# Kernel optimization log

Measured on AMD Instinct MI355X. Metric: run time of the kernel, lower is better.

The kernel has to match this reference:

```python
import jax, jax.numpy as jnp
from jax import lax
import numpy as np

MAX_SELECT = 100
NMS_THRESH = 0.1
LINES_PER_BLOCK = 4
CHARS_PER_LINE = 1
BELONG_THRESH = 0.6
SCORE_THRESH = 0.1
SAMPLE_NUM = 10


def cxcywh_to_xyxy(b):
    cx, cy, w, h = jnp.split(b, 4, axis=-1)
    return jnp.concatenate([cx - 0.5 * w, cy - 0.5 * h, cx + 0.5 * w, cy + 0.5 * h], axis=-1)


def bezier_aabb(cp):
    # cp: [K, 8, 2] control points (two cubic beziers: top 0:4, bottom 4:8)
    t = jnp.linspace(0.0, 1.0, SAMPLE_NUM)[:, None]      # [S,1]
    ti = 1.0 - t
    basis = jnp.concatenate([ti ** 3, 3 * t * ti ** 2, 3 * t ** 2 * ti, t ** 3], axis=-1)  # [S,4]
    top = jnp.einsum('sf,kfd->ksd', basis, cp[:, 0:4, :])
    bot = jnp.einsum('sf,kfd->ksd', basis, cp[:, 4:8, :])
    pts = jnp.concatenate([top, bot], axis=1)            # [K, 2S, 2]
    return jnp.concatenate([pts.min(axis=1), pts.max(axis=1)], axis=-1)  # [K,4] = x1,y1,x2,y2


def nms_keep_mask(boxes, init_keep, thresh):
    # boxes already sorted by descending score (topk order); returns keep mask
    K = boxes.shape[0]
    area = (boxes[:, 2] - boxes[:, 0]) * (boxes[:, 3] - boxes[:, 1])
    tl = jnp.maximum(boxes[:, None, :2], boxes[None, :, :2])
    br = jnp.minimum(boxes[:, None, 2:], boxes[None, :, 2:])
    wh = jnp.clip(br - tl, 0.0)
    inter = wh[..., 0] * wh[..., 1]
    iou = inter / (area[:, None] + area[None, :] - inter)
    idx = jnp.arange(K)

    def body(keep, i):
        sup = (iou[i] > thresh) & (idx > i) & keep[i]
        return keep & ~sup, None

    keep, _ = lax.scan(body, init_keep, jnp.arange(K))
    return keep


def filter_image(probs, raw, tsize, parent_raw, ef, is_bezier):
    # probs: [N], raw: [N, 4 or 16], tsize: [2] = (h, w)
    img_h, img_w = tsize[0], tsize[1]
    scale_box = jnp.stack([img_w, img_h, img_w, img_h])
    K = MAX_SELECT
    vals, sidx = lax.top_k(probs, K)
    keep = vals > SCORE_THRESH
    keep = jnp.where(keep.any(), keep, jnp.arange(K) == 0)

    if is_bezier:
        scale_pts = jnp.tile(tsize, 8)                    # [h,w]*8, matches repeat(8)
        ctrl = (raw[sidx] * scale_pts).reshape(K, 8, 2)
        boxes = bezier_aabb(ctrl)
        data = ctrl
    else:
        data = cxcywh_to_xyxy(raw[sidx]) * scale_box
        boxes = data

    if parent_raw is not None:
        pbox = cxcywh_to_xyxy(parent_raw[sidx // ef]) * scale_box
        ix1 = jnp.maximum(boxes[:, 0], pbox[:, 0])
        iy1 = jnp.maximum(boxes[:, 1], pbox[:, 1])
        ix2 = jnp.minimum(boxes[:, 2], pbox[:, 2])
        iy2 = jnp.minimum(boxes[:, 3], pbox[:, 3])
        inter = jnp.clip(ix2 - ix1, 0.0) * jnp.clip(iy2 - iy1, 0.0)
        carea = (boxes[:, 2] - boxes[:, 0]) * (boxes[:, 3] - boxes[:, 1])
        belong = inter / (carea + 1e-6)
        valid = belong > BELONG_THRESH
        fb = jnp.arange(K) == jnp.argmax(jnp.where(keep, belong, -jnp.inf))
        valid = jnp.where((valid & keep).any(), valid, fb)
        mask = keep & valid
    else:
        maxs = jnp.stack([img_w, img_h, img_w, img_h])
        data = jnp.clip(data, 0.0, maxs)
        boxes = data
        mask = keep

    nk = nms_keep_mask(lax.stop_gradient(boxes), mask, NMS_THRESH)
    if is_bezier:
        data = data.reshape(K, 16)
    data = jnp.where(nk[:, None], data, 0.0)
    scores = jnp.where(nk, vals, 0.0)
    return data, scores, nk


def _probs(logits):
    return jax.nn.sigmoid(logits)[..., 0]


def reference(pred_block_logits, pred_line_logits, pred_char_logits,
              pred_block, pred_line, pred_char, target_sizes):
    bp = _probs(pred_block_logits)
    lp = _probs(pred_line_logits)
    cp = _probs(pred_char_logits)
    blk = jax.vmap(lambda p, r, t: filter_image(p, r, t, None, 1, False))(bp, pred_block, target_sizes)
    lin = jax.vmap(lambda p, r, pr, t: filter_image(p, r, t, pr, LINES_PER_BLOCK, False))(lp, pred_line, pred_block, target_sizes)
    chr_ = jax.vmap(lambda p, r, pr, t: filter_image(p, r, t, pr, CHARS_PER_LINE, True))(cp, pred_char, pred_line, target_sizes)
    # padded outputs: (data, scores, keep_mask) per level; invalid rows are zeroed
    return (*blk, *lin, *chr_)


def setup_inputs() -> dict:
    key = jax.random.key(0)
    ks = jax.random.split(key, 7)
    B, NB, NL, NC = 64, 4096, 16384, 16384
    return {
        'pred_block_logits': jax.random.normal(ks[0], (B, NB, 1), jnp.float32),
        'pred_line_logits': jax.random.normal(ks[1], (B, NL, 1), jnp.float32),
        'pred_char_logits': jax.random.normal(ks[2], (B, NC, 1), jnp.float32),
        'pred_block': jax.random.uniform(ks[3], (B, NB, 4), jnp.float32),
        'pred_line': jax.random.uniform(ks[4], (B, NL, 4), jnp.float32),
        'pred_char': jax.random.uniform(ks[5], (B, NC, 16), jnp.float32),
        'target_sizes': 512.0 + 1024.0 * jax.random.uniform(ks[6], (B, 2), jnp.float32),
    }
```

## Files before the change

kernel.cpp:

```cpp
#include <hip/hip_runtime.h>
#include <math.h>

#define NTHREADS 256
#define KSEL 100
#define NBINS 2048
#define CAP 1024
#define SCORE_TH 0.1f
#define NMS_TH 0.1f
#define BELONG_TH 0.6f

typedef unsigned long long ull;

__device__ __forceinline__ ull make_key(float f, unsigned gidx) {
    unsigned u = __float_as_uint(f);
    u = (u & 0x80000000u) ? ~u : (u | 0x80000000u);
    return (((ull)u) << 32) | (ull)(0xFFFFFFFFu - gidx);
}
__device__ __forceinline__ float key_val(ull k) {
    unsigned u = (unsigned)(k >> 32);
    u = (u & 0x80000000u) ? (u ^ 0x80000000u) : ~u;
    return __uint_as_float(u);
}
__device__ __forceinline__ unsigned key_idx(ull k) {
    return 0xFFFFFFFFu - (unsigned)(k & 0xFFFFFFFFu);
}
__device__ __forceinline__ int binof(float p) {
    int b = (int)(p * (float)NBINS);
    b = b < 0 ? 0 : (b > NBINS - 1 ? NBINS - 1 : b);
    return b;
}

struct SharedMem {
    union {
        unsigned hist[NBINS];
        ull cand[CAP];
        ull part[4];
    } u;
    int bstar;
    int scnt;
    int wsum[4];
    float prob[KSEL];
    int   sidx[KSEL];
    float box[KSEL][4];
    float data16[KSEL][16];
    float area[KSEL];
    float belong[KSEL];
    unsigned char keep[KSEL];
    unsigned char valid[KSEL];
    unsigned char nk[KSEL];
    int argm;
    int anyvk;
};

template <int NPT, bool IS_BEZIER, bool HAS_PARENT>
__device__ void filter_impl(SharedMem* sm,
                            const float* __restrict__ logits,
                            const float* __restrict__ raw,
                            const float* __restrict__ parent_raw,
                            const float* __restrict__ tsizes,
                            float* __restrict__ out_data,
                            float* __restrict__ out_scores,
                            float* __restrict__ out_keep,
                            int img, int N, int PN, int ef) {
    const int tid = threadIdx.x;
    const int lane = tid & 63;
    const int wv = tid >> 6;
    const float* lg = logits + (size_t)img * N;

    for (int i = tid; i < NBINS; i += NTHREADS) sm->u.hist[i] = 0;
    if (tid == 0) sm->scnt = 0;
    __syncthreads();

    float p[NPT];
#pragma unroll
    for (int j = 0; j < NPT; ++j) {
        float x = lg[j * NTHREADS + tid];
        p[j] = 1.0f / (1.0f + expf(-x));
    }

#pragma unroll
    for (int j = 0; j < NPT; ++j)
        atomicAdd(&sm->u.hist[binof(p[j])], 1u);
    __syncthreads();

    int c[8];
    int s = 0;
#pragma unroll
    for (int q = 0; q < 8; ++q) {
        c[q] = (int)sm->u.hist[NBINS - 1 - 8 * tid - q];
        s += c[q];
    }
    int vv = s;
#pragma unroll
    for (int off = 1; off < 64; off <<= 1) {
        int o = __shfl_up(vv, off, 64);
        if (lane >= off) vv += o;
    }
    if (lane == 63) sm->wsum[wv] = vv;
    __syncthreads();
    int base = 0;
    for (int u2 = 0; u2 < wv; ++u2) base += sm->wsum[u2];
    int run = base + vv - s;
#pragma unroll
    for (int q = 0; q < 8; ++q) {
        int before = run;
        run += c[q];
        if (before < KSEL && run >= KSEL) sm->bstar = NBINS - 1 - 8 * tid - q;
    }
    __syncthreads();
    const int bstar = sm->bstar;

#pragma unroll
    for (int j = 0; j < NPT; ++j) {
        if (binof(p[j]) >= bstar) {
            int pos = atomicAdd(&sm->scnt, 1);
            if (pos < CAP) sm->u.cand[pos] = make_key(p[j], (unsigned)(j * NTHREADS + tid));
        }
    }
    __syncthreads();
    const int cnt = sm->scnt;

    if (cnt <= CAP) {
        for (int t = tid; t < cnt; t += NTHREADS) {
            ull mk = sm->u.cand[t];
            int rank = 0;
            for (int u2 = 0; u2 < cnt; ++u2) rank += (sm->u.cand[u2] > mk) ? 1 : 0;
            if (rank < KSEL) {
                sm->prob[rank] = key_val(mk);
                sm->sidx[rank] = (int)key_idx(mk);
            }
        }
    } else {
        ull best = make_key(p[0], (unsigned)tid);
#pragma unroll
        for (int j = 1; j < NPT; ++j) {
            ull kk = make_key(p[j], (unsigned)(j * NTHREADS + tid));
            if (kk > best) best = kk;
        }
        for (int k = 0; k < KSEL; ++k) {
            ull m = best;
#pragma unroll
            for (int off = 32; off > 0; off >>= 1) {
                ull o = __shfl_down(m, off, 64);
                if (o > m) m = o;
            }
            if (lane == 0) sm->u.part[wv] = m;
            __syncthreads();
            ull w = sm->u.part[0];
#pragma unroll
            for (int q = 1; q < 4; ++q)
                if (sm->u.part[q] > w) w = sm->u.part[q];
            if (tid == 0) {
                sm->prob[k] = key_val(w);
                sm->sidx[k] = (int)key_idx(w);
            }
            __syncthreads();
            unsigned gidx = key_idx(w);
            if ((gidx & (NTHREADS - 1)) == (unsigned)tid) {
                int j = (int)(gidx >> 8);
#pragma unroll
                for (int jj = 0; jj < NPT; ++jj)
                    if (jj == j) p[jj] = -INFINITY;
                best = make_key(p[0], (unsigned)tid);
#pragma unroll
                for (int jj = 1; jj < NPT; ++jj) {
                    ull kk = make_key(p[jj], (unsigned)(jj * NTHREADS + tid));
                    if (kk > best) best = kk;
                }
            }
        }
    }
    __syncthreads();

    const float Himg = tsizes[img * 2 + 0];
    const float Wimg = tsizes[img * 2 + 1];

    if (tid < KSEL) {
        const int k = tid;
        const int si = sm->sidx[k];
        const float val = sm->prob[k];
        const bool any = sm->prob[0] > SCORE_TH;
        bool keep = any ? (val > SCORE_TH) : (k == 0);

        float bx1, by1, bx2, by2;
        if (IS_BEZIER) {
            const float* r = raw + ((size_t)img * N + si) * 16;
            float c16[16];
#pragma unroll
            for (int mm = 0; mm < 8; ++mm) {
                c16[2 * mm]     = r[2 * mm]     * Himg;
                c16[2 * mm + 1] = r[2 * mm + 1] * Wimg;
            }
            float mn0 = INFINITY, mn1 = INFINITY, mx0 = -INFINITY, mx1 = -INFINITY;
            const float step = 1.0f / 9.0f;
#pragma unroll
            for (int sNum = 0; sNum < 10; ++sNum) {
                float t = (float)sNum * step;
                float ti = 1.0f - t;
                float b0 = ti * ti * ti;
                float b1 = 3.0f * t * ti * ti;
                float b2 = 3.0f * t * t * ti;
                float b3 = t * t * t;
#pragma unroll
                for (int cu = 0; cu < 2; ++cu) {
                    const float* cc = c16 + cu * 8;
                    float p0 = b0 * cc[0] + b1 * cc[2] + b2 * cc[4] + b3 * cc[6];
                    float p1 = b0 * cc[1] + b1 * cc[3] + b2 * cc[5] + b3 * cc[7];
                    mn0 = fminf(mn0, p0); mx0 = fmaxf(mx0, p0);
                    mn1 = fminf(mn1, p1); mx1 = fmaxf(mx1, p1);
                }
            }
            bx1 = mn0; by1 = mn1; bx2 = mx0; by2 = mx1;
#pragma unroll
            for (int mm = 0; mm < 16; ++mm) sm->data16[k][mm] = c16[mm];
        } else {
            const float* r = raw + ((size_t)img * N + si) * 4;
            float cx = r[0], cy = r[1], w = r[2], h = r[3];
            bx1 = (cx - 0.5f * w) * Wimg;
            by1 = (cy - 0.5f * h) * Himg;
            bx2 = (cx + 0.5f * w) * Wimg;
            by2 = (cy + 0.5f * h) * Himg;
            if (!HAS_PARENT) {
                bx1 = fminf(fmaxf(bx1, 0.0f), Wimg);
                by1 = fminf(fmaxf(by1, 0.0f), Himg);
                bx2 = fminf(fmaxf(bx2, 0.0f), Wimg);
                by2 = fminf(fmaxf(by2, 0.0f), Himg);
            }
        }
        sm->box[k][0] = bx1; sm->box[k][1] = by1;
        sm->box[k][2] = bx2; sm->box[k][3] = by2;
        sm->area[k] = (bx2 - bx1) * (by2 - by1);
        sm->keep[k] = keep ? 1 : 0;

        if (HAS_PARENT) {
            int pi = si / ef;
            const float* pr = parent_raw + ((size_t)img * PN + pi) * 4;
            float pcx = pr[0], pcy = pr[1], pw = pr[2], ph = pr[3];
            float px1 = (pcx - 0.5f * pw) * Wimg;
            float py1 = (pcy - 0.5f * ph) * Himg;
            float px2 = (pcx + 0.5f * pw) * Wimg;
            float py2 = (pcy + 0.5f * ph) * Himg;
            float ix1 = fmaxf(bx1, px1), iy1 = fmaxf(by1, py1);
            float ix2 = fminf(bx2, px2), iy2 = fminf(by2, py2);
            float inter = fmaxf(ix2 - ix1, 0.0f) * fmaxf(iy2 - iy1, 0.0f);
            float carea = (bx2 - bx1) * (by2 - by1);
            float belong = inter / (carea + 1e-6f);
            sm->belong[k] = belong;
            sm->valid[k] = (belong > BELONG_TH) ? 1 : 0;
        }
    }
    __syncthreads();

    if (HAS_PARENT) {
        if (tid < 64) {
            ull k0 = make_key(sm->keep[tid] ? sm->belong[tid] : -INFINITY, (unsigned)tid);
            bool p0 = sm->valid[tid] && sm->keep[tid];
            ull k1 = 0;
            bool p1 = false;
            if (tid < KSEL - 64) {
                k1 = make_key(sm->keep[tid + 64] ? sm->belong[tid + 64] : -INFINITY,
                              (unsigned)(tid + 64));
                p1 = sm->valid[tid + 64] && sm->keep[tid + 64];
            }
            ull m = k0 > k1 ? k0 : k1;
#pragma unroll
            for (int off = 32; off > 0; off >>= 1) {
                ull o = __shfl_xor(m, off, 64);
                if (o > m) m = o;
            }
            ull bal = __ballot(p0 || p1);
            if (lane == 0) {
                sm->argm = (int)key_idx(m);
                sm->anyvk = (bal != 0ULL) ? 1 : 0;
            }
        }
        __syncthreads();
        if (tid < KSEL) {
            bool valid = sm->anyvk ? (sm->valid[tid] != 0) : (tid == sm->argm);
            sm->nk[tid] = (sm->keep[tid] && valid) ? 1 : 0;
        }
    } else {
        if (tid < KSEL) sm->nk[tid] = sm->keep[tid];
    }
    __syncthreads();

    if (tid < 64) {
        const int l = tid;
        float s0x1 = sm->box[l][0], s0y1 = sm->box[l][1];
        float s0x2 = sm->box[l][2], s0y2 = sm->box[l][3];
        float s0a = sm->area[l];
        float s1x1 = 0.f, s1y1 = 0.f, s1x2 = 0.f, s1y2 = 0.f, s1a = 0.f;
        if (l < KSEL - 64) {
            s1x1 = sm->box[l + 64][0]; s1y1 = sm->box[l + 64][1];
            s1x2 = sm->box[l + 64][2]; s1y2 = sm->box[l + 64][3];
            s1a = sm->area[l + 64];
        }
        ull keepLo = __ballot(sm->nk[l] != 0);
        ull keepHi = __ballot((l < KSEL - 64) && (sm->nk[l + 64] != 0));
        for (int i = 0; i < KSEL; ++i) {
            bool ki = (i < 64) ? (((keepLo >> i) & 1ULL) != 0)
                               : (((keepHi >> (i - 64)) & 1ULL) != 0);
            if (!ki) continue;
            float bx1, by1, bx2, by2, ba;
            if (i < 64) {
                bx1 = __shfl(s0x1, i, 64); by1 = __shfl(s0y1, i, 64);
                bx2 = __shfl(s0x2, i, 64); by2 = __shfl(s0y2, i, 64);
                ba = __shfl(s0a, i, 64);
            } else {
                int ii = i - 64;
                bx1 = __shfl(s1x1, ii, 64); by1 = __shfl(s1y1, ii, 64);
                bx2 = __shfl(s1x2, ii, 64); by2 = __shfl(s1y2, ii, 64);
                ba = __shfl(s1a, ii, 64);
            }
            float ix1 = fmaxf(bx1, s0x1), iy1 = fmaxf(by1, s0y1);
            float ix2 = fminf(bx2, s0x2), iy2 = fminf(by2, s0y2);
            float in0 = fmaxf(ix2 - ix1, 0.0f) * fmaxf(iy2 - iy1, 0.0f);
            float iou0 = in0 / (ba + s0a - in0);
            bool sup0 = (l > i) && (iou0 > NMS_TH);
            float jx1 = fmaxf(bx1, s1x1), jy1 = fmaxf(by1, s1y1);
            float jx2 = fminf(bx2, s1x2), jy2 = fminf(by2, s1y2);
            float in1 = fmaxf(jx2 - jx1, 0.0f) * fmaxf(jy2 - jy1, 0.0f);
            float iou1 = in1 / (ba + s1a - in1);
            bool sup1 = ((l + 64) > i) && (iou1 > NMS_TH);
            keepLo &= ~__ballot(sup0);
            keepHi &= ~__ballot(sup1);
        }
        sm->nk[l] = (unsigned char)((keepLo >> l) & 1ULL);
        if (l < KSEL - 64) sm->nk[l + 64] = (unsigned char)((keepHi >> l) & 1ULL);
    }
    __syncthreads();

    if (tid < KSEL) {
        const int k = tid;
        const bool nk = sm->nk[k] != 0;
        out_scores[(size_t)img * KSEL + k] = nk ? sm->prob[k] : 0.0f;
        out_keep[(size_t)img * KSEL + k] = nk ? 1.0f : 0.0f;
        if (IS_BEZIER) {
#pragma unroll
            for (int mm = 0; mm < 16; ++mm)
                out_data[((size_t)img * KSEL + k) * 16 + mm] = nk ? sm->data16[k][mm] : 0.0f;
        } else {
#pragma unroll
            for (int mm = 0; mm < 4; ++mm)
                out_data[((size_t)img * KSEL + k) * 4 + mm] = nk ? sm->box[k][mm] : 0.0f;
        }
    }
}

__global__ __launch_bounds__(NTHREADS) void postprocess_kernel(
    const float* __restrict__ blk_logits, const float* __restrict__ lin_logits,
    const float* __restrict__ chr_logits, const float* __restrict__ blk_raw,
    const float* __restrict__ lin_raw, const float* __restrict__ chr_raw,
    const float* __restrict__ tsizes, float* __restrict__ out) {
    __shared__ SharedMem sm;
    const int b = blockIdx.x;
    const int level = b >> 6;
    const int img = b & 63;

    float* blk_data = out + 0;
    float* blk_sc   = out + 25600;
    float* blk_kp   = out + 32000;
    float* lin_data = out + 38400;
    float* lin_sc   = out + 64000;
    float* lin_kp   = out + 70400;
    float* chr_data = out + 76800;
    float* chr_sc   = out + 179200;
    float* chr_kp   = out + 185600;

    if (level == 0) {
        filter_impl<16, false, false>(&sm, blk_logits, blk_raw, nullptr, tsizes,
                                      blk_data, blk_sc, blk_kp, img, 4096, 0, 1);
    } else if (level == 1) {
        filter_impl<64, false, true>(&sm, lin_logits, lin_raw, blk_raw, tsizes,
                                     lin_data, lin_sc, lin_kp, img, 16384, 4096, 4);
    } else {
        filter_impl<64, true, true>(&sm, chr_logits, chr_raw, lin_raw, tsizes,
                                    chr_data, chr_sc, chr_kp, img, 16384, 16384, 1);
    }
}

extern "C" void kernel_launch(void* const* d_in, const int* in_sizes, int n_in,
                              void* d_out, int out_size, void* d_ws, size_t ws_size,
                              hipStream_t stream) {
    (void)in_sizes; (void)n_in; (void)d_ws; (void)ws_size; (void)out_size;
    const float* blk_logits = (const float*)d_in[0];
    const float* lin_logits = (const float*)d_in[1];
    const float* chr_logits = (const float*)d_in[2];
    const float* blk_raw = (const float*)d_in[3];
    const float* lin_raw = (const float*)d_in[4];
    const float* chr_raw = (const float*)d_in[5];
    const float* tsz = (const float*)d_in[6];
    float* out = (float*)d_out;

    hipLaunchKernelGGL(postprocess_kernel, dim3(192), dim3(NTHREADS), 0, stream,
                       blk_logits, lin_logits, chr_logits, blk_raw, lin_raw,
                       chr_raw, tsz, out);
}
```

Before: 134.4 us.

## Use 1024-thread blocks, vectorize loads, and precompute NMS suppression bitmasks in parallel

Raises the block size from 256 to 1024 threads, so each thread holds 4x fewer logits. Logits and box rows are read as float4, which means a new element-to-index mapping. NMS now computes the full pairwise IoU suppression bitmask in parallel across 16 waves into shared memory. A single wave then runs a cheap serial pass over those bitmasks instead of computing IoUs inside the serial loop. This targets latency in a grid of only 192 blocks, at the cost of extra syncs across 16 waves and a 16-way partial reduction in the rare fallback top-k path.

After: 131.8 us. 1.02x faster.

```diff
diff --git a/kernel.cpp b/kernel.cpp
--- a/kernel.cpp
+++ b/kernel.cpp
@@ -1,7 +1,8 @@
 #include <hip/hip_runtime.h>
 #include <math.h>
 
-#define NTHREADS 256
+#define NTHREADS 1024
+#define NWAVES 16
 #define KSEL 100
 #define NBINS 2048
 #define CAP 1024
@@ -29,22 +30,26 @@
     b = b < 0 ? 0 : (b > NBINS - 1 ? NBINS - 1 : b);
     return b;
 }
+__device__ __forceinline__ unsigned gidx_of(int e, int tid) {
+    return ((unsigned)(e >> 2)) * (NTHREADS * 4) + ((unsigned)tid << 2) + (unsigned)(e & 3);
+}
 
 struct SharedMem {
     union {
         unsigned hist[NBINS];
         ull cand[CAP];
-        ull part[4];
+        ull part[NWAVES];
     } u;
     int bstar;
     int scnt;
-    int wsum[4];
+    int wsum[NWAVES];
     float prob[KSEL];
     int   sidx[KSEL];
-    float box[KSEL][4];
+    alignas(16) float box[KSEL][4];
     float data16[KSEL][16];
     float area[KSEL];
     float belong[KSEL];
+    ull nmsrow[KSEL][2];
     unsigned char keep[KSEL];
     unsigned char valid[KSEL];
     unsigned char nk[KSEL];
@@ -67,15 +72,20 @@
     const int wv = tid >> 6;
     const float* lg = logits + (size_t)img * N;
 
+#pragma unroll
     for (int i = tid; i < NBINS; i += NTHREADS) sm->u.hist[i] = 0;
     if (tid == 0) sm->scnt = 0;
     __syncthreads();
 
     float p[NPT];
-#pragma unroll
-    for (int j = 0; j < NPT; ++j) {
-        float x = lg[j * NTHREADS + tid];
-        p[j] = 1.0f / (1.0f + expf(-x));
+    const float4* lg4 = (const float4*)lg;
+#pragma unroll
+    for (int v = 0; v < NPT / 4; ++v) {
+        float4 x = lg4[v * NTHREADS + tid];
+        p[4 * v + 0] = 1.0f / (1.0f + expf(-x.x));
+        p[4 * v + 1] = 1.0f / (1.0f + expf(-x.y));
+        p[4 * v + 2] = 1.0f / (1.0f + expf(-x.z));
+        p[4 * v + 3] = 1.0f / (1.0f + expf(-x.w));
     }
 
 #pragma unroll
@@ -83,13 +93,9 @@
         atomicAdd(&sm->u.hist[binof(p[j])], 1u);
     __syncthreads();
 
-    int c[8];
-    int s = 0;
-#pragma unroll
-    for (int q = 0; q < 8; ++q) {
-        c[q] = (int)sm->u.hist[NBINS - 1 - 8 * tid - q];
-        s += c[q];
-    }
+    int c0 = (int)sm->u.hist[NBINS - 1 - 2 * tid];
+    int c1 = (int)sm->u.hist[NBINS - 2 - 2 * tid];
+    int s = c0 + c1;
     int vv = s;
 #pragma unroll
     for (int off = 1; off < 64; off <<= 1) {
@@ -99,14 +105,12 @@
     if (lane == 63) sm->wsum[wv] = vv;
     __syncthreads();
     int base = 0;
-    for (int u2 = 0; u2 < wv; ++u2) base += sm->wsum[u2];
+#pragma unroll
+    for (int u2 = 0; u2 < NWAVES; ++u2) base += (u2 < wv) ? sm->wsum[u2] : 0;
     int run = base + vv - s;
-#pragma unroll
-    for (int q = 0; q < 8; ++q) {
-        int before = run;
-        run += c[q];
-        if (before < KSEL && run >= KSEL) sm->bstar = NBINS - 1 - 8 * tid - q;
-    }
+    if (run < KSEL && run + c0 >= KSEL) sm->bstar = NBINS - 1 - 2 * tid;
+    int run2 = run + c0;
+    if (run2 < KSEL && run2 + c1 >= KSEL) sm->bstar = NBINS - 2 - 2 * tid;
     __syncthreads();
     const int bstar = sm->bstar;
 
@@ -114,7 +118,7 @@
     for (int j = 0; j < NPT; ++j) {
         if (binof(p[j]) >= bstar) {
             int pos = atomicAdd(&sm->scnt, 1);
-            if (pos < CAP) sm->u.cand[pos] = make_key(p[j], (unsigned)(j * NTHREADS + tid));
+            if (pos < CAP) sm->u.cand[pos] = make_key(p[j], gidx_of(j, tid));
         }
     }
     __syncthreads();
@@ -131,10 +135,10 @@
             }
         }
     } else {
-        ull best = make_key(p[0], (unsigned)tid);
+        ull best = make_key(p[0], gidx_of(0, tid));
 #pragma unroll
         for (int j = 1; j < NPT; ++j) {
-            ull kk = make_key(p[j], (unsigned)(j * NTHREADS + tid));
+            ull kk = make_key(p[j], gidx_of(j, tid));
             if (kk > best) best = kk;
         }
         for (int k = 0; k < KSEL; ++k) {
@@ -148,7 +152,7 @@
             __syncthreads();
             ull w = sm->u.part[0];
 #pragma unroll
-            for (int q = 1; q < 4; ++q)
+            for (int q = 1; q < NWAVES; ++q)
                 if (sm->u.part[q] > w) w = sm->u.part[q];
             if (tid == 0) {
                 sm->prob[k] = key_val(w);
@@ -156,15 +160,15 @@
             }
             __syncthreads();
             unsigned gidx = key_idx(w);
-            if ((gidx & (NTHREADS - 1)) == (unsigned)tid) {
-                int j = (int)(gidx >> 8);
+            if (((gidx >> 2) & (NTHREADS - 1)) == (unsigned)tid) {
+                int e = (int)(((gidx >> 12) << 2) | (gidx & 3));
 #pragma unroll
                 for (int jj = 0; jj < NPT; ++jj)
-                    if (jj == j) p[jj] = -INFINITY;
-                best = make_key(p[0], (unsigned)tid);
+                    if (jj == e) p[jj] = -INFINITY;
+                best = make_key(p[0], gidx_of(0, tid));
 #pragma unroll
                 for (int jj = 1; jj < NPT; ++jj) {
-                    ull kk = make_key(p[jj], (unsigned)(jj * NTHREADS + tid));
+                    ull kk = make_key(p[jj], gidx_of(jj, tid));
                     if (kk > best) best = kk;
                 }
             }
@@ -184,12 +188,15 @@
 
         float bx1, by1, bx2, by2;
         if (IS_BEZIER) {
-            const float* r = raw + ((size_t)img * N + si) * 16;
+            const float4* r4 = (const float4*)(raw + ((size_t)img * N + si) * 16);
             float c16[16];
 #pragma unroll
-            for (int mm = 0; mm < 8; ++mm) {
-                c16[2 * mm]     = r[2 * mm]     * Himg;
-                c16[2 * mm + 1] = r[2 * mm + 1] * Wimg;
+            for (int v = 0; v < 4; ++v) {
+                float4 x = r4[v];
+                c16[4 * v + 0] = x.x * Himg;
+                c16[4 * v + 1] = x.y * Wimg;
+                c16[4 * v + 2] = x.z * Himg;
+                c16[4 * v + 3] = x.w * Wimg;
             }
             float mn0 = INFINITY, mn1 = INFINITY, mx0 = -INFINITY, mx1 = -INFINITY;
             const float step = 1.0f / 9.0f;
@@ -214,8 +221,8 @@
 #pragma unroll
             for (int mm = 0; mm < 16; ++mm) sm->data16[k][mm] = c16[mm];
         } else {
-            const float* r = raw + ((size_t)img * N + si) * 4;
-            float cx = r[0], cy = r[1], w = r[2], h = r[3];
+            float4 r = *(const float4*)(raw + ((size_t)img * N + si) * 4);
+            float cx = r.x, cy = r.y, w = r.z, h = r.w;
             bx1 = (cx - 0.5f * w) * Wimg;
             by1 = (cy - 0.5f * h) * Himg;
             bx2 = (cx + 0.5f * w) * Wimg;
@@ -234,12 +241,11 @@
 
         if (HAS_PARENT) {
             int pi = si / ef;
-            const float* pr = parent_raw + ((size_t)img * PN + pi) * 4;
-            float pcx = pr[0], pcy = pr[1], pw = pr[2], ph = pr[3];
-            float px1 = (pcx - 0.5f * pw) * Wimg;
-            float py1 = (pcy - 0.5f * ph) * Himg;
-            float px2 = (pcx + 0.5f * pw) * Wimg;
-            float py2 = (pcy + 0.5f * ph) * Himg;
+            float4 pr = *(const float4*)(parent_raw + ((size_t)img * PN + pi) * 4);
+            float px1 = (pr.x - 0.5f * pr.z) * Wimg;
+            float py1 = (pr.y - 0.5f * pr.w) * Himg;
+            float px2 = (pr.x + 0.5f * pr.z) * Wimg;
+            float py2 = (pr.y + 0.5f * pr.w) * Himg;
             float ix1 = fmaxf(bx1, px1), iy1 = fmaxf(by1, py1);
             float ix2 = fminf(bx2, px2), iy2 = fminf(by2, py2);
             float inter = fmaxf(ix2 - ix1, 0.0f) * fmaxf(iy2 - iy1, 0.0f);
@@ -284,46 +290,58 @@
     }
     __syncthreads();
 
+    {
+        float4 b0 = *(const float4*)sm->box[lane];
+        float a0 = sm->area[lane];
+        float4 b1 = make_float4(0.f, 0.f, 0.f, 0.f);
+        float a1 = 0.f;
+        if (lane < KSEL - 64) {
+            b1 = *(const float4*)sm->box[lane + 64];
+            a1 = sm->area[lane + 64];
+        }
+        for (int i = wv; i < KSEL; i += NWAVES) {
+            float rx1, ry1, rx2, ry2, ra;
+            if (i < 64) {
+                rx1 = __shfl(b0.x, i, 64); ry1 = __shfl(b0.y, i, 64);
+                rx2 = __shfl(b0.z, i, 64); ry2 = __shfl(b0.w, i, 64);
+                ra  = __shfl(a0, i, 64);
+            } else {
+                rx1 = __shfl(b1.x, i - 64, 64); ry1 = __shfl(b1.y, i - 64, 64);
+                rx2 = __shfl(b1.z, i - 64, 64); ry2 = __shfl(b1.w, i - 64, 64);
+                ra  = __shfl(a1, i - 64, 64);
+            }
+            float ix1 = fmaxf(rx1, b0.x), iy1 = fmaxf(ry1, b0.y);
+            float ix2 = fminf(rx2, b0.z), iy2 = fminf(ry2, b0.w);
+            float in0 = fmaxf(ix2 - ix1, 0.0f) * fmaxf(iy2 - iy1, 0.0f);
+            float iou0 = in0 / (ra + a0 - in0);
+            bool sup0 = (lane > i) && (iou0 > NMS_TH);
+            float jx1 = fmaxf(rx1, b1.x), jy1 = fmaxf(ry1, b1.y);
+            float jx2 = fminf(rx2, b1.z), jy2 = fminf(ry2, b1.w);
+            float in1 = fmaxf(jx2 - jx1, 0.0f) * fmaxf(jy2 - jy1, 0.0f);
+            float iou1 = in1 / (ra + a1 - in1);
+            bool sup1 = (lane < KSEL - 64) && ((lane + 64) > i) && (iou1 > NMS_TH);
+            ull w0 = __ballot(sup0);
+            ull w1 = __ballot(sup1);
+            if (lane == 0) { sm->nmsrow[i][0] = w0; sm->nmsrow[i][1] = w1; }
+        }
+    }
+    __syncthreads();
+
     if (tid < 64) {
-        const int l = tid;
-        float s0x1 = sm->box[l][0], s0y1 = sm->box[l][1];
-        float s0x2 = sm->box[l][2], s0y2 = sm->box[l][3];
-        float s0a = sm->area[l];
-        float s1x1 = 0.f, s1y1 = 0.f, s1x2 = 0.f, s1y2 = 0.f, s1a = 0.f;
-        if (l < KSEL - 64) {
-            s1x1 = sm->box[l + 64][0]; s1y1 = sm->box[l + 64][1];
-            s1x2 = sm->box[l + 64][2]; s1y2 = sm->box[l + 64][3];
-            s1a = sm->area[l + 64];
-        }
+        const int l = lane;
+        ull r0lo = sm->nmsrow[l][0], r0hi = sm->nmsrow[l][1];
+        ull r1lo = 0, r1hi = 0;
+        if (l < KSEL - 64) { r1lo = sm->nmsrow[l + 64][0]; r1hi = sm->nmsrow[l + 64][1]; }
         ull keepLo = __ballot(sm->nk[l] != 0);
         ull keepHi = __ballot((l < KSEL - 64) && (sm->nk[l + 64] != 0));
+#pragma unroll
         for (int i = 0; i < KSEL; ++i) {
             bool ki = (i < 64) ? (((keepLo >> i) & 1ULL) != 0)
                                : (((keepHi >> (i - 64)) & 1ULL) != 0);
-            if (!ki) continue;
-            float bx1, by1, bx2, by2, ba;
-            if (i < 64) {
-                bx1 = __shfl(s0x1, i, 64); by1 = __shfl(s0y1, i, 64);
-                bx2 = __shfl(s0x2, i, 64); by2 = __shfl(s0y2, i, 64);
-                ba = __shfl(s0a, i, 64);
-            } else {
-                int ii = i - 64;
-                bx1 = __shfl(s1x1, ii, 64); by1 = __shfl(s1y1, ii, 64);
-                bx2 = __shfl(s1x2, ii, 64); by2 = __shfl(s1y2, ii, 64);
-                ba = __shfl(s1a, ii, 64);
-            }
-            float ix1 = fmaxf(bx1, s0x1), iy1 = fmaxf(by1, s0y1);
-            float ix2 = fminf(bx2, s0x2), iy2 = fminf(by2, s0y2);
-            float in0 = fmaxf(ix2 - ix1, 0.0f) * fmaxf(iy2 - iy1, 0.0f);
-            float iou0 = in0 / (ba + s0a - in0);
-            bool sup0 = (l > i) && (iou0 > NMS_TH);
-            float jx1 = fmaxf(bx1, s1x1), jy1 = fmaxf(by1, s1y1);
-            float jx2 = fminf(bx2, s1x2), jy2 = fminf(by2, s1y2);
-            float in1 = fmaxf(jx2 - jx1, 0.0f) * fmaxf(jy2 - jy1, 0.0f);
-            float iou1 = in1 / (ba + s1a - in1);
-            bool sup1 = ((l + 64) > i) && (iou1 > NMS_TH);
-            keepLo &= ~__ballot(sup0);
-            keepHi &= ~__ballot(sup1);
+            ull slo = (i < 64) ? __shfl(r0lo, i, 64) : __shfl(r1lo, i - 64, 64);
+            ull shi = (i < 64) ? __shfl(r0hi, i, 64) : __shfl(r1hi, i - 64, 64);
+            keepLo &= ki ? ~slo : ~0ULL;
+            keepHi &= ki ? ~shi : ~0ULL;
         }
         sm->nk[l] = (unsigned char)((keepLo >> l) & 1ULL);
         if (l < KSEL - 64) sm->nk[l + 64] = (unsigned char)((keepHi >> l) & 1ULL);
@@ -368,13 +386,13 @@
     float* chr_kp   = out + 185600;
 
     if (level == 0) {
-        filter_impl<16, false, false>(&sm, blk_logits, blk_raw, nullptr, tsizes,
-                                      blk_data, blk_sc, blk_kp, img, 4096, 0, 1);
+        filter_impl<4, false, false>(&sm, blk_logits, blk_raw, nullptr, tsizes,
+                                     blk_data, blk_sc, blk_kp, img, 4096, 0, 1);
     } else if (level == 1) {
-        filter_impl<64, false, true>(&sm, lin_logits, lin_raw, blk_raw, tsizes,
+        filter_impl<16, false, true>(&sm, lin_logits, lin_raw, blk_raw, tsizes,
                                      lin_data, lin_sc, lin_kp, img, 16384, 4096, 4);
     } else {
-        filter_impl<64, true, true>(&sm, chr_logits, chr_raw, lin_raw, tsizes,
+        filter_impl<16, true, true>(&sm, chr_logits, chr_raw, lin_raw, tsizes,
                                     chr_data, chr_sc, chr_kp, img, 16384, 16384, 1);
     }
 }
```
